# Kernel optimization log

Measured on AMD Instinct MI355X. Metric: run time of the kernel, lower is better.

## Reference

```python
import jax, jax.numpy as jnp
import numpy as np

SIZES = (1, 2, 4, 6)  # pooled tokens: 1+4+16+36 = 57


def setup_inputs() -> dict:
    key = jax.random.key(0)
    B, Cin, Cf, H, W = 8, 256, 256, 96, 96
    Np = sum(s * s for s in SIZES)  # 57
    keys = iter(jax.random.split(key, 48))

    def nrm(shape, s=0.05):
        return jax.random.normal(next(keys), shape, dtype=jnp.float32) * s

    d = dict(
        x1=nrm((B, Cin, H, W), 1.0), x2=nrm((B, Cin, H, W), 1.0),
        x3=nrm((B, Cf, H, W), 1.0), x4=nrm((B, Cf, H, W), 1.0),
        conv3_w=nrm((Cf, Cin, 1, 1)), conv3_b=nrm((Cf,)),
        bn3_g=jnp.ones((Cf,), jnp.float32), bn3_b=jnp.zeros((Cf,), jnp.float32), bn3_m=nrm((Cf,)), bn3_v=jnp.ones((Cf,), jnp.float32),
        conv4_w=nrm((Cf, Cin, 1, 1)), conv4_b=nrm((Cf,)),
        bn4_g=jnp.ones((Cf,), jnp.float32), bn4_b=jnp.zeros((Cf,), jnp.float32), bn4_m=nrm((Cf,)), bn4_v=jnp.ones((Cf,), jnp.float32),
        conv1_w=nrm((Cf, Cf, 3, 3)), conv1_b=nrm((Cf,)),
        bn1_g=jnp.ones((Cf,), jnp.float32), bn1_b=jnp.zeros((Cf,), jnp.float32), bn1_m=nrm((Cf,)), bn1_v=jnp.ones((Cf,), jnp.float32),
        conv2_w=nrm((Cf, Cf, 3, 3)), conv2_b=nrm((Cf,)),
        bn2_g=jnp.ones((Cf,), jnp.float32), bn2_b=jnp.zeros((Cf,), jnp.float32), bn2_m=nrm((Cf,)), bn2_v=jnp.ones((Cf,), jnp.float32),
        fc1_w=nrm((1, 4, 1, 1)), fc1_b=nrm((1,)),
        fc2_w=nrm((1, 4, 1, 1)), fc2_b=nrm((1,)),
        fc3_w1=nrm((16, Np, 1, 1)), fc3_b1=nrm((16,)), fc3_w2=nrm((1, 16, 1, 1)), fc3_b2=nrm((1,)),
    )
    return d


def _bn(x, g, be, m, v, eps=1e-5):
    # inference-mode BatchNorm2d
    return (x - m[None, :, None, None]) * (g * jax.lax.rsqrt(v + eps))[None, :, None, None] + be[None, :, None, None]


def _conv(x, w, b, pad):
    y = jax.lax.conv_general_dilated(x, w, (1, 1), [(pad, pad), (pad, pad)],
                                     dimension_numbers=('NCHW', 'OIHW', 'NCHW'))
    return y + b[None, :, None, None]


def _transform(x, s):
    # adaptive_avg_pool2d to (s, s) as exact block mean (H, W divisible by s)
    b, c, H, W = x.shape
    p = x.reshape(b, c, s, H // s, s, W // s).mean(axis=(3, 5))
    return p.reshape(b, c, s * s).transpose(0, 2, 1)  # (b, s*s, c)


def reference(x1, x2, x3, x4,
              conv3_w, conv3_b, bn3_g, bn3_b, bn3_m, bn3_v,
              conv4_w, conv4_b, bn4_g, bn4_b, bn4_m, bn4_v,
              conv1_w, conv1_b, bn1_g, bn1_b, bn1_m, bn1_v,
              conv2_w, conv2_b, bn2_g, bn2_b, bn2_m, bn2_v,
              fc1_w, fc1_b, fc2_w, fc2_b,
              fc3_w1, fc3_b1, fc3_w2, fc3_b2):
    f1 = _bn(_conv(x1, conv3_w, conv3_b, 0), bn3_g, bn3_b, bn3_m, bn3_v)
    f2 = _bn(_conv(x2, conv4_w, conv4_b, 0), bn4_g, bn4_b, bn4_m, bn4_v)

    y1 = jnp.concatenate([_transform(f1, s) for s in SIZES], axis=1)  # (b, 57, Cf)
    y2 = jnp.concatenate([_transform(f2, s) for s in SIZES], axis=1)
    y1 = y1 / jnp.maximum(jnp.linalg.norm(y1, axis=-1, keepdims=True), 1e-12)
    y2 = y2 / jnp.maximum(jnp.linalg.norm(y2, axis=-1, keepdims=True), 1e-12)

    s1 = 1.0 - jnp.einsum('bnc,bmc->bnm', y1, y1)
    s2 = 1.0 - jnp.einsum('bnc,bmc->bnm', y2, y2)
    s12 = 1.0 - jnp.einsum('bnc,bmc->bnm', y1, y2)
    a = jnp.stack([s1, s2, s1 * s2, s12], axis=1)  # (b, 4, 57, 57)

    a1 = jax.nn.softmax(jnp.einsum('bknm,k->bnm', a, fc1_w.reshape(4)) + fc1_b[0], axis=-1)
    a2 = jax.nn.softmax(jnp.einsum('bknm,k->bnm', a, fc2_w.reshape(4)) + fc2_b[0], axis=-1)

    g1 = jnp.einsum('bnm,bmc->bnc', a1, y1)  # (b, 57, Cf)
    g2 = jnp.einsum('bnm,bmc->bnc', a2, y2)

    def fc3(g):
        # original code applies fc3 to BOTH branches (fc4 is unused)
        h = jnp.einsum('bnc,kn->bkc', g, fc3_w1.reshape(16, -1)) + fc3_b1[None, :, None]
        o = jnp.einsum('bkc,k->bc', h, fc3_w2.reshape(16)) + fc3_b2[0]
        return jax.nn.sigmoid(o)[:, :, None, None]  # (b, Cf, 1, 1)

    gate1 = fc3(g1)
    gate2 = fc3(g2)

    x3_out = x3 + gate1 * _bn(_conv(x4, conv1_w, conv1_b, 1), bn1_g, bn1_b, bn1_m, bn1_v)
    x4_out = x4 + gate2 * _bn(_conv(x3, conv2_w, conv2_b, 1), bn2_g, bn2_b, bn2_m, bn2_v)
    return (x3_out, x4_out)
```

## Files before the change

### kernel.cpp

```cpp
#include <hip/hip_runtime.h>


#define BATCH 8
#define CH    256
#define HH    96
#define WW    96
#define HWA   9216
#define NP    57
#define PH    98
#define KTOT  2304
#define NCHUNK 72
#define OUTHALF (BATCH*CH*HWA)
#define YSTR  260

typedef short  short8  __attribute__((ext_vector_type(8)));
typedef float  float4f __attribute__((ext_vector_type(4)));
typedef unsigned short us4 __attribute__((ext_vector_type(4)));

__device__ __forceinline__ unsigned short f2bf(float f) {
    unsigned int u = __float_as_uint(f);
    u += 0x7fffu + ((u >> 16) & 1u);
    return (unsigned short)(u >> 16);
}

#define GLDS16(gp, sp) __builtin_amdgcn_global_load_lds( \
    (const __attribute__((address_space(1))) void*)(gp),  \
    (__attribute__((address_space(3))) void*)(sp), 16, 0, 0)

__global__ void pool_kernel(const float* __restrict__ x1,
                            const float* __restrict__ x2,
                            float* __restrict__ px) {
    int c = blockIdx.x, b = blockIdx.y, z = blockIdx.z;
    const float* src = (z ? x2 : x1) + ((long)b * CH + c) * HWA;
    __shared__ float seg[1152];
    __shared__ float bins[144];
    int t = threadIdx.x;
    for (int s = t; s < 1152; s += 256) {
        int r = s / 12, cb = s - r * 12;
        const float4f* p = (const float4f*)(src + r * 96 + cb * 8);
        float4f a = p[0], bv = p[1];
        seg[s] = (a.x + a.y) + (a.z + a.w) + (bv.x + bv.y) + (bv.z + bv.w);
    }
    __syncthreads();
    if (t < 144) {
        int i = t / 12, j = t - i * 12;
        float s = 0.f;
#pragma unroll
        for (int r = 0; r < 8; ++r) s += seg[(i * 8 + r) * 12 + j];
        bins[t] = s;
    }
    __syncthreads();
    if (t < NP) {
        int bh0, bw0, nb;
        if (t == 0)      { bh0 = 0; bw0 = 0; nb = 12; }
        else if (t < 5)  { int q = t - 1;  bh0 = (q >> 1) * 6; bw0 = (q & 1) * 6; nb = 6; }
        else if (t < 21) { int q = t - 5;  bh0 = (q >> 2) * 3; bw0 = (q & 3) * 3; nb = 3; }
        else             { int q = t - 21; bh0 = (q / 6) * 2;  bw0 = (q % 6) * 2; nb = 2; }
        float s = 0.f;
        for (int i = 0; i < nb; ++i)
            for (int j = 0; j < nb; ++j)
                s += bins[(bh0 + i) * 12 + (bw0 + j)];
        px[(((long)z * BATCH + b) * CH + c) * NP + t] = s / (float)(nb * nb * 64);
    }
}

__global__ void ycomp_kernel(const float* __restrict__ px,
    const float* __restrict__ w3, const float* __restrict__ cb3,
    const float* __restrict__ g3, const float* __restrict__ be3,
    const float* __restrict__ m3, const float* __restrict__ v3,
    const float* __restrict__ w4, const float* __restrict__ cb4,
    const float* __restrict__ g4, const float* __restrict__ be4,
    const float* __restrict__ m4, const float* __restrict__ v4,
    float* __restrict__ y) {
    int n = blockIdx.x, b = blockIdx.y, z = blockIdx.z;
    __shared__ float col[CH];
    __shared__ float red[CH];
    int c = threadIdx.x;
    col[c] = px[(((long)z * BATCH + b) * CH + c) * NP + n];
    __syncthreads();
    const float* w  = z ? w4  : w3;
    const float* cb = z ? cb4 : cb3;
    const float* gg = z ? g4  : g3;
    const float* be = z ? be4 : be3;
    const float* mm = z ? m4  : m3;
    const float* vv = z ? v4  : v3;
    float s = gg[c] * rsqrtf(vv[c] + 1e-5f);
    const float4f* wr4  = (const float4f*)(w + (long)c * CH);
    const float4f* col4 = (const float4f*)col;
    float4f a4 = {0.f, 0.f, 0.f, 0.f};
#pragma unroll 8
    for (int ci = 0; ci < CH / 4; ++ci) a4 += wr4[ci] * col4[ci];
    float acc = (a4.x + a4.y) + (a4.z + a4.w);
    float yv = s * acc + (cb[c] - mm[c]) * s + be[c];
    red[c] = yv * yv;
    __syncthreads();
    for (int st = 128; st > 0; st >>= 1) {
        if (c < st) red[c] += red[c + st];
        __syncthreads();
    }
    float scale = 1.f / fmaxf(sqrtf(red[0]), 1e-12f);
    y[(((long)z * BATCH + b) * NP + n) * CH + c] = yv * scale;
}

__global__ void attn_kernel(const float* __restrict__ y,
    const float* __restrict__ fw1, const float* __restrict__ fb1,
    const float* __restrict__ fw2, const float* __restrict__ fb2,
    const float* __restrict__ w31, const float* __restrict__ b31,
    const float* __restrict__ w32, const float* __restrict__ b32,
    float* __restrict__ gates) {
    int b = blockIdx.x, t = threadIdx.x;
    __shared__ __align__(16) float y1s[NP * YSTR];
    __shared__ __align__(16) float y2s[NP * YSTR];
    __shared__ float l1[NP * NP];
    __shared__ float l2[NP * NP];
    __shared__ float w31s[16 * NP];
    __shared__ float W21[16 * NP];
    __shared__ float W22[16 * NP];
    const float* y1g = y + (long)b * NP * CH;
    const float* y2g = y + (long)(BATCH + b) * NP * CH;
    for (int i = t; i < NP * 64; i += 256) {
        int n = i >> 6, cq = i & 63;
        *(float4f*)&y1s[n * YSTR + cq * 4] = *(const float4f*)&y1g[n * CH + cq * 4];
        *(float4f*)&y2s[n * YSTR + cq * 4] = *(const float4f*)&y2g[n * CH + cq * 4];
    }
    for (int i = t; i < 16 * NP; i += 256) w31s[i] = w31[i];
    __syncthreads();
    float a10 = fw1[0], a11 = fw1[1], a12 = fw1[2], a13 = fw1[3], b1v = fb1[0];
    float a20 = fw2[0], a21 = fw2[1], a22 = fw2[2], a23 = fw2[3], b2v = fb2[0];
    int p0 = (t & 7) * 8;
    for (int idx = t; idx < NP * NP; idx += 256) {
        int n = idx / NP, m = idx - n * NP;
        const float4f* yn1 = (const float4f*)&y1s[n * YSTR];
        const float4f* ym1 = (const float4f*)&y1s[m * YSTR];
        const float4f* yn2 = (const float4f*)&y2s[n * YSTR];
        const float4f* ym2 = (const float4f*)&y2s[m * YSTR];
        float4f d1 = {0,0,0,0}, d2 = {0,0,0,0}, d12 = {0,0,0,0};
        for (int q = 0; q < 64; ++q) {
            int cq = (q + p0) & 63;
            float4f a1 = yn1[cq], bb1 = ym1[cq];
            float4f a2 = yn2[cq], bb2 = ym2[cq];
            d1 += a1 * bb1; d2 += a2 * bb2; d12 += a1 * bb2;
        }
        float dd1 = (d1.x + d1.y) + (d1.z + d1.w);
        float dd2 = (d2.x + d2.y) + (d2.z + d2.w);
        float dd12 = (d12.x + d12.y) + (d12.z + d12.w);
        float s1 = 1.f - dd1, s2 = 1.f - dd2, s12 = 1.f - dd12;
        l1[idx] = a10 * s1 + a11 * s2 + a12 * s1 * s2 + a13 * s12 + b1v;
        l2[idx] = a20 * s1 + a21 * s2 + a22 * s1 * s2 + a23 * s12 + b2v;
    }
    __syncthreads();
    if (t < 2 * NP) {
        int which = t >= NP;
        int n = which ? t - NP : t;
        float* l = which ? l2 : l1;
        float mx = -1e30f;
        for (int m = 0; m < NP; ++m) mx = fmaxf(mx, l[n * NP + m]);
        float sum = 0.f;
        for (int m = 0; m < NP; ++m) { float e = __expf(l[n * NP + m] - mx); l[n * NP + m] = e; sum += e; }
        float inv = 1.f / sum;
        for (int m = 0; m < NP; ++m) l[n * NP + m] *= inv;
    }
    __syncthreads();
    for (int i = t; i < 16 * NP; i += 256) {
        int k = i / NP, m = i - k * NP;
        float s1 = 0.f, s2 = 0.f;
        for (int n = 0; n < NP; ++n) {
            float wv = w31s[k * NP + n];
            s1 += wv * l1[n * NP + m];
            s2 += wv * l2[n * NP + m];
        }
        W21[i] = s1; W22[i] = s2;
    }
    __syncthreads();
    int c = t;
    float h1[16], h2[16];
#pragma unroll
    for (int k = 0; k < 16; ++k) { h1[k] = 0.f; h2[k] = 0.f; }
    for (int m = 0; m < NP; ++m) {
        float ym1 = y1s[m * YSTR + c];
        float ym2 = y2s[m * YSTR + c];
#pragma unroll
        for (int k = 0; k < 16; ++k) {
            h1[k] += W21[k * NP + m] * ym1;
            h2[k] += W22[k * NP + m] * ym2;
        }
    }
    float o1 = b32[0], o2 = b32[0];
#pragma unroll
    for (int k = 0; k < 16; ++k) {
        float wk = w32[k];
        o1 += wk * (h1[k] + b31[k]);
        o2 += wk * (h2[k] + b31[k]);
    }
    gates[b * CH + c]        = 1.f / (1.f + __expf(-o1));
    gates[2048 + b * CH + c] = 1.f / (1.f + __expf(-o2));
}

__global__ void prepack_kernel(
    const float* __restrict__ w1, const float* __restrict__ cb1,
    const float* __restrict__ g1, const float* __restrict__ be1,
    const float* __restrict__ m1, const float* __restrict__ v1,
    const float* __restrict__ w2, const float* __restrict__ cb2,
    const float* __restrict__ g2, const float* __restrict__ be2,
    const float* __restrict__ m2, const float* __restrict__ v2,
    unsigned short* __restrict__ Wp, float* __restrict__ bias) {
    long idx = (long)blockIdx.x * 256 + threadIdx.x;
    int which = idx >= (long)CH * KTOT;
    long rem = idx - (long)which * CH * KTOT;
    int co = (int)(rem / KTOT);
    int k  = (int)(rem - (long)co * KTOT);
    int r = k >> 8, ci = k & 255;
    int dy = r / 3, dx = r - dy * 3;
    const float* w  = which ? w2  : w1;
    const float* cb = which ? cb2 : cb1;
    const float* gg = which ? g2  : g1;
    const float* be = which ? be2 : be1;
    const float* mm = which ? m2  : m1;
    const float* vv = which ? v2  : v1;
    float s = gg[co] * rsqrtf(vv[co] + 1e-5f);
    float val = w[(((long)co * CH + ci) * 3 + dy) * 3 + dx] * s;
    Wp[idx] = f2bf(val);
    if (k == 0) bias[which * CH + co] = (cb[co] - mm[co]) * s + be[co];
}

__global__ void pad_kernel(const float* __restrict__ x3,
                           const float* __restrict__ x4,
                           unsigned short* __restrict__ xp3,
                           unsigned short* __restrict__ xp4) {
    int hp = blockIdx.x, b = blockIdx.y, z = blockIdx.z;
    const float* src = z ? x4 : x3;
    unsigned short* dst = z ? xp4 : xp3;
    __shared__ float buf[64][97];
    int t = threadIdx.x;
    bool border = (hp == 0 || hp == PH - 1);
    int h = hp - 1;
    for (int ci0 = 0; ci0 < CH; ci0 += 64) {
        if (!border) {
            for (int idx = t; idx < 64 * 96; idx += 256) {
                int cl = idx / 96, w = idx - cl * 96;
                buf[cl][w] = src[(((long)b * CH + ci0 + cl) * HH + h) * WW + w];
            }
        }
        __syncthreads();
        for (int idx = t; idx < PH * 16; idx += 256) {
            int wp = idx >> 4, cq = idx & 15;
            us4 v = {0, 0, 0, 0};
            if (!border && wp >= 1 && wp <= 96) {
                int wq = wp - 1;
                v.x = f2bf(buf[cq * 4 + 0][wq]);
                v.y = f2bf(buf[cq * 4 + 1][wq]);
                v.z = f2bf(buf[cq * 4 + 2][wq]);
                v.w = f2bf(buf[cq * 4 + 3][wq]);
            }
            *(us4*)&dst[(((long)b * PH + hp) * PH + wp) * CH + ci0 + cq * 4] = v;
        }
        __syncthreads();
    }
}

__global__ __launch_bounds__(256, 2)
void conv_gemm(const unsigned short* __restrict__ xp3,
               const unsigned short* __restrict__ xp4,
               const unsigned short* __restrict__ Wp0,
               const float* __restrict__ gates,
               const float* __restrict__ bias2,
               const float* __restrict__ x3,
               const float* __restrict__ x4,
               float* __restrict__ outg) {
    int zc = blockIdx.y;
    const unsigned short* xp = zc ? xp3 : xp4;
    const unsigned short* Wp = Wp0 + (long)zc * CH * KTOT;
    const float* gate  = gates + (long)zc * 2048;
    const float* bias  = bias2 + zc * CH;
    const float* resid = zc ? x4 : x3;
    float* out = outg + (long)zc * OUTHALF;

    __shared__ short As[2][4 * 128 * 8];
    __shared__ short Bs[2][4 * 256 * 8];
    int tid = threadIdx.x;
    int bm0 = blockIdx.x;
    int bm = (bm0 & 7) * 72 + (bm0 >> 3);
    int bimg = bm / 72, tt = bm - bimg * 72;
    int h0 = (tt / 6) * 8, w0 = (tt % 6) * 16;

    int lane = tid & 63, wid = tid >> 6;
    int wm = wid & 1, wn = wid >> 1;
    int lm = lane & 15, quad = lane >> 4;

    long apix0 = ((long)(bimg * PH + h0 + (lane >> 4)) * PH + (w0 + (lane & 15))) * CH + wid * 8;
    long apix1 = ((long)(bimg * PH + h0 + 4 + (lane >> 4)) * PH + (w0 + (lane & 15))) * CH + wid * 8;
    long bb0 = (long)(lane) * KTOT + wid * 8;
    long bb1 = (long)(64 + lane) * KTOT + wid * 8;
    long bb2 = (long)(128 + lane) * KTOT + wid * 8;
    long bb3 = (long)(192 + lane) * KTOT + wid * 8;

    float4f acc[4][8] = {};

    auto STAGE = [&](int buf, int kc) {
        int r9 = kc >> 3;
        int dy = r9 / 3, dx = r9 - dy * 3;
        long aoff = (long)(dy * PH + dx) * CH + ((kc & 7) << 5);
        long boff = (long)kc << 5;
        short* asd = &As[buf][wid * 1024];
        short* bsd = &Bs[buf][wid * 2048];
        GLDS16(xp + apix0 + aoff, asd);
        GLDS16(xp + apix1 + aoff, asd + 512);
        GLDS16(Wp + bb0 + boff, bsd);
        GLDS16(Wp + bb1 + boff, bsd + 512);
        GLDS16(Wp + bb2 + boff, bsd + 1024);
        GLDS16(Wp + bb3 + boff, bsd + 1536);
    };

    STAGE(0, 0);
    STAGE(1, 1);
    int cur = 0;
    for (int kc = 0; kc < NCHUNK; ++kc) {
        if (kc + 1 < NCHUNK) {
            asm volatile("s_waitcnt vmcnt(6)\n\ts_barrier" ::: "memory");
        } else {
            asm volatile("s_waitcnt vmcnt(0)\n\ts_barrier" ::: "memory");
        }
        short8 af[4], bfr[8];
#pragma unroll
        for (int i = 0; i < 4; ++i)
            af[i] = *(short8*)&As[cur][quad * 1024 + (wm * 64 + i * 16 + lm) * 8];
#pragma unroll
        for (int j = 0; j < 8; ++j)
            bfr[j] = *(short8*)&Bs[cur][quad * 2048 + (wn * 128 + j * 16 + lm) * 8];
#pragma unroll
        for (int i = 0; i < 4; ++i)
#pragma unroll
            for (int j = 0; j < 8; ++j)
                acc[i][j] = __builtin_amdgcn_mfma_f32_16x16x32_bf16(af[i], bfr[j], acc[i][j], 0, 0, 0);
        asm volatile("s_waitcnt lgkmcnt(0)\n\ts_barrier" ::: "memory");
        if (kc + 2 < NCHUNK) STAGE(cur, kc + 2);
        cur ^= 1;
    }

#pragma unroll
    for (int j = 0; j < 8; ++j) {
        int co = wn * 128 + j * 16 + lm;
        float g  = gate[bimg * CH + co];
        float bv = bias[co];
#pragma unroll
        for (int i = 0; i < 4; ++i) {
            int h = h0 + wm * 4 + i;
            int w = w0 + quad * 4;
            long o = ((long)(bimg * CH + co)) * HWA + h * WW + w;
            float4f rv = *(const float4f*)(resid + o);
            float4f ov = rv + g * (acc[i][j] + bv);
            *(float4f*)(out + o) = ov;
        }
    }
}

extern "C" void kernel_launch(void* const* d_in, const int* in_sizes, int n_in,
                              void* d_out, int out_size, void* d_ws, size_t ws_size,
                              hipStream_t stream) {
    const float* x1 = (const float*)d_in[0];
    const float* x2 = (const float*)d_in[1];
    const float* x3 = (const float*)d_in[2];
    const float* x4 = (const float*)d_in[3];
    const float* conv3_w = (const float*)d_in[4];
    const float* conv3_b = (const float*)d_in[5];
    const float* bn3_g = (const float*)d_in[6];
    const float* bn3_b = (const float*)d_in[7];
    const float* bn3_m = (const float*)d_in[8];
    const float* bn3_v = (const float*)d_in[9];
    const float* conv4_w = (const float*)d_in[10];
    const float* conv4_b = (const float*)d_in[11];
    const float* bn4_g = (const float*)d_in[12];
    const float* bn4_b = (const float*)d_in[13];
    const float* bn4_m = (const float*)d_in[14];
    const float* bn4_v = (const float*)d_in[15];
    const float* conv1_w = (const float*)d_in[16];
    const float* conv1_b = (const float*)d_in[17];
    const float* bn1_g = (const float*)d_in[18];
    const float* bn1_b = (const float*)d_in[19];
    const float* bn1_m = (const float*)d_in[20];
    const float* bn1_v = (const float*)d_in[21];
    const float* conv2_w = (const float*)d_in[22];
    const float* conv2_b = (const float*)d_in[23];
    const float* bn2_g = (const float*)d_in[24];
    const float* bn2_b = (const float*)d_in[25];
    const float* bn2_m = (const float*)d_in[26];
    const float* bn2_v = (const float*)d_in[27];
    const float* fc1_w = (const float*)d_in[28];
    const float* fc1_b = (const float*)d_in[29];
    const float* fc2_w = (const float*)d_in[30];
    const float* fc2_b = (const float*)d_in[31];
    const float* fc3_w1 = (const float*)d_in[32];
    const float* fc3_b1 = (const float*)d_in[33];
    const float* fc3_w2 = (const float*)d_in[34];
    const float* fc3_b2 = (const float*)d_in[35];

    float* ws = (float*)d_ws;
    float* px    = ws;
    float* y     = ws + 233472;
    float* gates = ws + 466944;
    float* bias  = ws + 471040;
    unsigned short* Wp  = (unsigned short*)(ws + 471552);
    unsigned short* xp3 = Wp + 2 * CH * KTOT;
    unsigned short* xp4 = xp3 + (long)BATCH * PH * PH * CH;

    pool_kernel<<<dim3(256, 8, 2), 256, 0, stream>>>(x1, x2, px);
    ycomp_kernel<<<dim3(57, 8, 2), 256, 0, stream>>>(px,
        conv3_w, conv3_b, bn3_g, bn3_b, bn3_m, bn3_v,
        conv4_w, conv4_b, bn4_g, bn4_b, bn4_m, bn4_v, y);
    attn_kernel<<<dim3(8), 256, 0, stream>>>(y, fc1_w, fc1_b, fc2_w, fc2_b,
        fc3_w1, fc3_b1, fc3_w2, fc3_b2, gates);
    prepack_kernel<<<dim3(4608), 256, 0, stream>>>(
        conv1_w, conv1_b, bn1_g, bn1_b, bn1_m, bn1_v,
        conv2_w, conv2_b, bn2_g, bn2_b, bn2_m, bn2_v, Wp, bias);
    pad_kernel<<<dim3(PH, 8, 2), 256, 0, stream>>>(x3, x4, xp3, xp4);

    conv_gemm<<<dim3(576, 2), 256, 0, stream>>>(xp3, xp4, Wp, gates, bias,
        x3, x4, (float*)d_out);
}
```

Measured before the change: 930.1 us.

## Repack padded activations and weights into chunk-blocked layouts for coalesced LDS loads

The padded bf16 activation buffer moves from NHWC to a channel-group-of-8 blocked layout (b, cgroup, h, w, 8). The packed weights are reordered so each K-chunk's 256x32 tile sits contiguously in exactly the order the GEMM writes to LDS. This turns the global-to-LDS loads into contiguous runs instead of strided rows, which should improve coalescing and cache line use in the conv GEMM. The pad kernel now writes 16-byte vectors in the new layout, and the prepack index math changes to match.

```diff
diff --git a/kernel.cpp b/kernel.cpp
--- a/kernel.cpp
+++ b/kernel.cpp
@@ -12,10 +12,12 @@
 #define NCHUNK 72
 #define OUTHALF (BATCH*CH*HWA)
 #define YSTR  260
+#define XPP   (PH*PH*8)
 
 typedef short  short8  __attribute__((ext_vector_type(8)));
 typedef float  float4f __attribute__((ext_vector_type(4)));
 typedef unsigned short us4 __attribute__((ext_vector_type(4)));
+typedef unsigned short us8 __attribute__((ext_vector_type(8)));
 
 __device__ __forceinline__ unsigned short f2bf(float f) {
     unsigned int u = __float_as_uint(f);
@@ -207,9 +209,14 @@
     long idx = (long)blockIdx.x * 256 + threadIdx.x;
     int which = idx >= (long)CH * KTOT;
     long rem = idx - (long)which * CH * KTOT;
-    int co = (int)(rem / KTOT);
-    int k  = (int)(rem - (long)co * KTOT);
-    int r = k >> 8, ci = k & 255;
+    int kc   = (int)(rem >> 13);
+    int r2   = (int)(rem & 8191);
+    int quad = r2 >> 11;
+    int r3   = r2 & 2047;
+    int co   = r3 >> 3;
+    int e    = r3 & 7;
+    int cb_  = kc & 7, r = kc >> 3;
+    int ci   = cb_ * 32 + quad * 8 + e;
     int dy = r / 3, dx = r - dy * 3;
     const float* w  = which ? w2  : w1;
     const float* cb = which ? cb2 : cb1;
@@ -220,7 +227,8 @@
     float s = gg[co] * rsqrtf(vv[co] + 1e-5f);
     float val = w[(((long)co * CH + ci) * 3 + dy) * 3 + dx] * s;
     Wp[idx] = f2bf(val);
-    if (k == 0) bias[which * CH + co] = (cb[co] - mm[co]) * s + be[co];
+    if (kc == 0 && quad == 0 && e == 0)
+        bias[which * CH + co] = (cb[co] - mm[co]) * s + be[co];
 }
 
 __global__ void pad_kernel(const float* __restrict__ x3,
@@ -242,17 +250,16 @@
             }
         }
         __syncthreads();
-        for (int idx = t; idx < PH * 16; idx += 256) {
-            int wp = idx >> 4, cq = idx & 15;
-            us4 v = {0, 0, 0, 0};
+        for (int idx = t; idx < 8 * PH; idx += 256) {
+            int cg = idx / PH, wp = idx - cg * PH;
+            us8 v = {0, 0, 0, 0, 0, 0, 0, 0};
             if (!border && wp >= 1 && wp <= 96) {
                 int wq = wp - 1;
-                v.x = f2bf(buf[cq * 4 + 0][wq]);
-                v.y = f2bf(buf[cq * 4 + 1][wq]);
-                v.z = f2bf(buf[cq * 4 + 2][wq]);
-                v.w = f2bf(buf[cq * 4 + 3][wq]);
+#pragma unroll
+                for (int j = 0; j < 8; ++j) v[j] = f2bf(buf[cg * 8 + j][wq]);
             }
-            *(us4*)&dst[(((long)b * PH + hp) * PH + wp) * CH + ci0 + cq * 4] = v;
+            long o = (((long)b * 32 + (ci0 >> 3) + cg) * PH + hp) * PH + wp;
+            *(us8*)&dst[o * 8] = v;
         }
         __syncthreads();
     }
@@ -287,28 +294,25 @@
     int wm = wid & 1, wn = wid >> 1;
     int lm = lane & 15, quad = lane >> 4;
 
-    long apix0 = ((long)(bimg * PH + h0 + (lane >> 4)) * PH + (w0 + (lane & 15))) * CH + wid * 8;
-    long apix1 = ((long)(bimg * PH + h0 + 4 + (lane >> 4)) * PH + (w0 + (lane & 15))) * CH + wid * 8;
-    long bb0 = (long)(lane) * KTOT + wid * 8;
-    long bb1 = (long)(64 + lane) * KTOT + wid * 8;
-    long bb2 = (long)(128 + lane) * KTOT + wid * 8;
-    long bb3 = (long)(192 + lane) * KTOT + wid * 8;
+    long apix0 = ((((long)bimg * 32 + wid) * PH + (h0 + (lane >> 4))) * PH + (w0 + (lane & 15))) * 8;
+    long apix1 = apix0 + (long)4 * PH * 8;
+    long bbase = (long)wid * 2048 + (long)lane * 8;
 
     float4f acc[4][8] = {};
 
     auto STAGE = [&](int buf, int kc) {
         int r9 = kc >> 3;
         int dy = r9 / 3, dx = r9 - dy * 3;
-        long aoff = (long)(dy * PH + dx) * CH + ((kc & 7) << 5);
-        long boff = (long)kc << 5;
+        long aoff = (long)(kc & 7) * 4 * XPP + (long)(dy * PH + dx) * 8;
+        long boff = (long)kc * 8192 + bbase;
         short* asd = &As[buf][wid * 1024];
         short* bsd = &Bs[buf][wid * 2048];
         GLDS16(xp + apix0 + aoff, asd);
         GLDS16(xp + apix1 + aoff, asd + 512);
-        GLDS16(Wp + bb0 + boff, bsd);
-        GLDS16(Wp + bb1 + boff, bsd + 512);
-        GLDS16(Wp + bb2 + boff, bsd + 1024);
-        GLDS16(Wp + bb3 + boff, bsd + 1536);
+        GLDS16(Wp + boff,        bsd);
+        GLDS16(Wp + boff + 512,  bsd + 512);
+        GLDS16(Wp + boff + 1024, bsd + 1024);
+        GLDS16(Wp + boff + 1536, bsd + 1536);
     };
 
     STAGE(0, 0);
@@ -401,7 +405,7 @@
     float* bias  = ws + 471040;
     unsigned short* Wp  = (unsigned short*)(ws + 471552);
     unsigned short* xp3 = Wp + 2 * CH * KTOT;
-    unsigned short* xp4 = xp3 + (long)BATCH * PH * PH * CH;
+    unsigned short* xp4 = xp3 + (long)BATCH * 32 * XPP;
 
     pool_kernel<<<dim3(256, 8, 2), 256, 0, stream>>>(x1, x2, px);
     ycomp_kernel<<<dim3(57, 8, 2), 256, 0, stream>>>(px,
```

Result: faster. 815.0 us (-12.4%).
